# Performance work log

Measured on AMD Instinct MI355X. Metric: run time of the kernel, lower is better.

The kernel has to match this reference:

```python
import jax, jax.numpy as jnp
import numpy as np

WEIGHT = 0.01
EPS = 1e-12  # torch F.normalize default eps


def setup_inputs() -> dict:
    key = jax.random.key(0)
    factor = jax.random.normal(key, (65536, 2048), dtype=jnp.float32)
    return {"factor": factor}


def reference(factor):
    # L2-normalize rows (torch F.normalize, dim=1): x / max(||x||, eps)
    norms = jnp.linalg.norm(factor, axis=1, keepdims=True)
    f = factor / jnp.maximum(norms, EPS)
    N = f.shape[0]
    # diag(f @ f.T, +1)[i] = <f_i, f_{i+1}>; diag(.., -1) is identical by symmetry.
    adj = jnp.sum(f[:-1] * f[1:], axis=1)  # [N-1]
    positive1 = jnp.sum(adj) / (N - 1)
    positive2 = positive1  # gram matrix is symmetric
    time_diff = positive1 + positive2
    return -WEIGHT * time_diff
```

## Files before the change

kernel.cpp:

```cpp
#include <hip/hip_runtime.h>
#include <math.h>


#define N_ROWS 65536
#define N_COLS 2048
#define ROWS_PER_WAVE 16

__global__ __launch_bounds__(256) void tcr_pass1(const float* __restrict__ x,
                                                 float* __restrict__ sq,
                                                 float* __restrict__ cross) {
    const int wid  = (blockIdx.x * 256 + threadIdx.x) >> 6;
    const int lane = threadIdx.x & 63;
    const long r0 = (long)wid * ROWS_PER_WAVE;

    const float4* rowp = (const float4*)x;

    float4 prev[8];
    {
        long base = r0 * 512 + lane;
        #pragma unroll
        for (int k = 0; k < 8; ++k) prev[k] = rowp[base + (long)k * 64];
    }
    {
        float s = 0.f;
        #pragma unroll
        for (int k = 0; k < 8; ++k)
            s += prev[k].x * prev[k].x + prev[k].y * prev[k].y +
                 prev[k].z * prev[k].z + prev[k].w * prev[k].w;
        #pragma unroll
        for (int off = 32; off; off >>= 1) s += __shfl_xor(s, off, 64);
        if (lane == 0) sq[r0] = s;
    }

    const int rend = (int)r0 + ROWS_PER_WAVE;
    for (int r = (int)r0 + 1; r <= rend; ++r) {
        if (r >= N_ROWS) break;
        float4 cur[8];
        long base = (long)r * 512 + lane;
        #pragma unroll
        for (int k = 0; k < 8; ++k) cur[k] = rowp[base + (long)k * 64];

        float sqp = 0.f, crp = 0.f;
        #pragma unroll
        for (int k = 0; k < 8; ++k) {
            sqp += cur[k].x * cur[k].x + cur[k].y * cur[k].y +
                   cur[k].z * cur[k].z + cur[k].w * cur[k].w;
            crp += prev[k].x * cur[k].x + prev[k].y * cur[k].y +
                   prev[k].z * cur[k].z + prev[k].w * cur[k].w;
            prev[k] = cur[k];
        }
        #pragma unroll
        for (int off = 32; off; off >>= 1) {
            sqp += __shfl_xor(sqp, off, 64);
            crp += __shfl_xor(crp, off, 64);
        }
        if (lane == 0) {
            cross[r - 1] = crp;
            if (r < rend) sq[r] = sqp;
        }
    }
}

__global__ __launch_bounds__(256) void tcr_pass2(const float* __restrict__ sq,
                                                 const float* __restrict__ cross,
                                                 float* __restrict__ out) {
    const int tid    = blockIdx.x * 256 + threadIdx.x;
    const int stride = gridDim.x * 256;
    double acc = 0.0;
    for (int i = tid; i < N_ROWS - 1; i += stride) {
        double ni = fmax(sqrt((double)sq[i]),     1e-12);
        double nj = fmax(sqrt((double)sq[i + 1]), 1e-12);
        acc += (double)cross[i] / (ni * nj);
    }
    __shared__ double sd[256];
    sd[threadIdx.x] = acc;
    __syncthreads();
    for (int s = 128; s; s >>= 1) {
        if (threadIdx.x < s) sd[threadIdx.x] += sd[threadIdx.x + s];
        __syncthreads();
    }
    if (threadIdx.x == 0) {
        double partial = sd[0] * (-2.0 * 0.01 / (double)(N_ROWS - 1));
        atomicAdd(out, (float)partial);
    }
}

extern "C" void kernel_launch(void* const* d_in, const int* in_sizes, int n_in,
                              void* d_out, int out_size, void* d_ws, size_t ws_size,
                              hipStream_t stream) {
    const float* factor = (const float*)d_in[0];
    float* out = (float*)d_out;

    float* sq    = (float*)d_ws;
    float* cross = sq + N_ROWS;

    const int n_waves  = N_ROWS / ROWS_PER_WAVE;
    const int n_blocks = n_waves / 4;
    tcr_pass1<<<n_blocks, 256, 0, stream>>>(factor, sq, cross);

    hipMemsetAsync(d_out, 0, sizeof(float), stream);

    tcr_pass2<<<64, 256, 0, stream>>>(sq, cross, out);
}
```

Measured before the change: 686.4 us.

## Give each wave two rows with all loads issued up front instead of serial streaming

The first pass now gives each wave two rows plus the next row, instead of walking 16 rows one after another. All 24 float4 loads per lane are issued before any arithmetic, and the grid grows eightfold. This targets the latency-bound serial load chain in the old loop and the low number of resident waves. In exchange, each row is fetched about 1.5 times on average; the extra fetch is the neighbouring wave's row and may be served from cache.

```diff
diff --git a/kernel.cpp b/kernel.cpp
--- a/kernel.cpp
+++ b/kernel.cpp
@@ -4,60 +4,56 @@
 
 #define N_ROWS 65536
 #define N_COLS 2048
-#define ROWS_PER_WAVE 16
+
+typedef float v4f __attribute__((ext_vector_type(4)));
 
 __global__ __launch_bounds__(256) void tcr_pass1(const float* __restrict__ x,
                                                  float* __restrict__ sq,
                                                  float* __restrict__ cross) {
     const int wid  = (blockIdx.x * 256 + threadIdx.x) >> 6;
     const int lane = threadIdx.x & 63;
-    const long r0 = (long)wid * ROWS_PER_WAVE;
+    const int r0   = wid * 2;
+    const v4f* __restrict__ rowp = (const v4f*)x;
 
-    const float4* rowp = (const float4*)x;
+    int r2 = r0 + 2; if (r2 > N_ROWS - 1) r2 = N_ROWS - 1;
 
-    float4 prev[8];
-    {
-        long base = r0 * 512 + lane;
-        #pragma unroll
-        for (int k = 0; k < 8; ++k) prev[k] = rowp[base + (long)k * 64];
+    const long bA = (long)r0 * 512 + lane;
+    const long bB = bA + 512;
+    const long bC = (long)r2 * 512 + lane;
+
+    v4f A[8], B[8], C[8];
+    #pragma unroll
+    for (int k = 0; k < 8; ++k) A[k] = rowp[bA + k * 64];
+    #pragma unroll
+    for (int k = 0; k < 8; ++k) B[k] = rowp[bB + k * 64];
+    #pragma unroll
+    for (int k = 0; k < 8; ++k) C[k] = rowp[bC + k * 64];
+
+    float s0 = 0.f, c0 = 0.f;
+    #pragma unroll
+    for (int k = 0; k < 8; ++k) {
+        s0 += A[k].x * A[k].x + A[k].y * A[k].y + A[k].z * A[k].z + A[k].w * A[k].w;
+        c0 += A[k].x * B[k].x + A[k].y * B[k].y + A[k].z * B[k].z + A[k].w * B[k].w;
     }
-    {
-        float s = 0.f;
-        #pragma unroll
-        for (int k = 0; k < 8; ++k)
-            s += prev[k].x * prev[k].x + prev[k].y * prev[k].y +
-                 prev[k].z * prev[k].z + prev[k].w * prev[k].w;
-        #pragma unroll
-        for (int off = 32; off; off >>= 1) s += __shfl_xor(s, off, 64);
-        if (lane == 0) sq[r0] = s;
+    float s1 = 0.f, c1 = 0.f;
+    #pragma unroll
+    for (int k = 0; k < 8; ++k) {
+        s1 += B[k].x * B[k].x + B[k].y * B[k].y + B[k].z * B[k].z + B[k].w * B[k].w;
+        c1 += B[k].x * C[k].x + B[k].y * C[k].y + B[k].z * C[k].z + B[k].w * C[k].w;
     }
 
-    const int rend = (int)r0 + ROWS_PER_WAVE;
-    for (int r = (int)r0 + 1; r <= rend; ++r) {
-        if (r >= N_ROWS) break;
-        float4 cur[8];
-        long base = (long)r * 512 + lane;
-        #pragma unroll
-        for (int k = 0; k < 8; ++k) cur[k] = rowp[base + (long)k * 64];
-
-        float sqp = 0.f, crp = 0.f;
-        #pragma unroll
-        for (int k = 0; k < 8; ++k) {
-            sqp += cur[k].x * cur[k].x + cur[k].y * cur[k].y +
-                   cur[k].z * cur[k].z + cur[k].w * cur[k].w;
-            crp += prev[k].x * cur[k].x + prev[k].y * cur[k].y +
-                   prev[k].z * cur[k].z + prev[k].w * cur[k].w;
-            prev[k] = cur[k];
-        }
-        #pragma unroll
-        for (int off = 32; off; off >>= 1) {
-            sqp += __shfl_xor(sqp, off, 64);
-            crp += __shfl_xor(crp, off, 64);
-        }
-        if (lane == 0) {
-            cross[r - 1] = crp;
-            if (r < rend) sq[r] = sqp;
-        }
+    #pragma unroll
+    for (int off = 32; off; off >>= 1) {
+        s0 += __shfl_xor(s0, off, 64);
+        c0 += __shfl_xor(c0, off, 64);
+        s1 += __shfl_xor(s1, off, 64);
+        c1 += __shfl_xor(c1, off, 64);
+    }
+    if (lane == 0) {
+        sq[r0]        = s0;
+        sq[r0 + 1]    = s1;
+        cross[r0]     = c0;
+        cross[r0 + 1] = c1;
     }
 }
 
@@ -94,8 +90,7 @@
     float* sq    = (float*)d_ws;
     float* cross = sq + N_ROWS;
 
-    const int n_waves  = N_ROWS / ROWS_PER_WAVE;
-    const int n_blocks = n_waves / 4;
+    const int n_blocks = (N_ROWS / 2) / 4;
     tcr_pass1<<<n_blocks, 256, 0, stream>>>(factor, sq, cross);
 
     hipMemsetAsync(d_out, 0, sizeof(float), stream);
```

Result: no change. 675.8 us (-1.5%).
